# Performance work log

Hardware: AMD Instinct MI355X
Metric: run time of the kernel (lower is better)

## Reference

```python
import jax, jax.numpy as jnp
import numpy as np

DIM = 256
WH, WW = 7, 7
N = WH * WW
HEADS = 8
HEAD_DIM = DIM // HEADS
SCALE = HEAD_DIM ** -0.5
B_ = 4096
NW = 64  # windows per image; B_ % NW == 0


def _relative_position_index():
    coords = np.stack(np.meshgrid(np.arange(WH), np.arange(WW), indexing='ij'))  # (2,Wh,Ww)
    flat = coords.reshape(2, -1)  # (2,N)
    rel = flat[:, :, None] - flat[:, None, :]  # (2,N,N)
    rel = rel.transpose(1, 2, 0)  # (N,N,2)
    rel = rel + np.array([WH - 1, WW - 1])
    rel = rel * np.array([2 * WW - 1, 1])
    return rel.sum(-1).astype(np.int32)  # (N,N)


def setup_inputs() -> dict:
    key = jax.random.key(0)
    ks = jax.random.split(key, 7)
    num_rel = (2 * WH - 1) * (2 * WW - 1)
    return {
        'x': jax.random.normal(ks[0], (B_, N, DIM), jnp.float32),
        'mask': jax.random.normal(ks[1], (NW, N, N), jnp.float32),
        'qkv_w': jax.random.normal(ks[2], (DIM, 3 * DIM), jnp.float32) * 0.02,
        'qkv_b': jnp.zeros((3 * DIM,), jnp.float32),
        'proj_w': jax.random.normal(ks[3], (DIM, DIM), jnp.float32) * 0.02,
        'proj_b': jnp.zeros((DIM,), jnp.float32),
        'bias_table': jax.random.normal(ks[4], (num_rel, HEADS), jnp.float32) * 0.02,
        'rel_index': jnp.asarray(_relative_position_index()),
    }


def reference(x, mask, qkv_w, qkv_b, proj_w, proj_b, bias_table, rel_index):
    B, n, C = x.shape
    qkv = x @ qkv_w + qkv_b  # (B,N,3C)
    qkv = qkv.reshape(B, n, 3, HEADS, HEAD_DIM).transpose(2, 0, 3, 1, 4)
    q, k, v = qkv[0], qkv[1], qkv[2]  # (B,H,N,hd)
    attn = jnp.einsum('bhnd,bhmd->bhnm', q * SCALE, k)  # (B,H,N,N)
    rel_bias = bias_table[rel_index.reshape(-1)].reshape(n, n, HEADS)
    attn = attn + rel_bias.transpose(2, 0, 1)[None]  # (B,H,N,N)
    nW = mask.shape[0]
    attn = attn.reshape(-1, nW, HEADS, n, n) + mask[None, :, None]
    attn = attn.reshape(-1, HEADS, n, n)
    attn = jax.nn.softmax(attn, axis=-1)
    out = jnp.einsum('bhnm,bhmd->bhnd', attn, v)  # (B,H,N,hd)
    out = out.transpose(0, 2, 1, 3).reshape(B, n, C)
    return out @ proj_w + proj_b
```

## Files before the change

### kernel.cpp

```cpp
#include <hip/hip_runtime.h>
#include <hip/hip_bf16.h>


#define NTOK 49
static constexpr float SCALE_Q = 0.17677669529663687f;

using bf16   = __bf16;
using bf16x4 = __attribute__((ext_vector_type(4))) __bf16;
using bf16x8 = __attribute__((ext_vector_type(8))) __bf16;
using short4v = __attribute__((ext_vector_type(4))) short;
using f32x4  = __attribute__((ext_vector_type(4))) float;

#define WT_QKV_OFF 0
#define WT_PROJ_OFF (768 * 256 * 2)
#define SB_OFF (WT_PROJ_OFF + 256 * 256 * 2)
#define SM_OFF (SB_OFF + 8 * 4096 * 4)
#define WS_NEEDED (SM_OFF + (size_t)64 * 4096 * 4)

static __device__ __forceinline__ f32x4 mfma16(bf16x4 a, bf16x4 b, f32x4 c) {
#if __has_builtin(__builtin_amdgcn_mfma_f32_16x16x16_bf16)
    return __builtin_amdgcn_mfma_f32_16x16x16_bf16(a, b, c, 0, 0, 0);
#elif __has_builtin(__builtin_amdgcn_mfma_f32_16x16x16bf16_1k)
    return __builtin_amdgcn_mfma_f32_16x16x16bf16_1k(
        __builtin_bit_cast(short4v, a), __builtin_bit_cast(short4v, b), c, 0, 0, 0);
#elif __has_builtin(__builtin_amdgcn_mfma_f32_16x16x16_bf16_1k)
    return __builtin_amdgcn_mfma_f32_16x16x16_bf16_1k(
        __builtin_bit_cast(short4v, a), __builtin_bit_cast(short4v, b), c, 0, 0, 0);
#else
    asm volatile("v_mfma_f32_16x16x16_bf16 %0, %1, %2, %0\n\t"
                 "s_nop 7\n\ts_nop 7\n\ts_nop 1"
                 : "+v"(c) : "v"(a), "v"(b));
    return c;
#endif
}

static __device__ __forceinline__ bf16x8 ldsA(const char* base, int row, int koff) {
    return *(const bf16x8*)(base + row * 512 + (koff ^ ((row & 7) << 4)));
}
static __device__ __forceinline__ bf16x8 ldB(const bf16* wt, int ncol, int k2, int hf, int g) {
    return *(const bf16x8*)(wt + ncol * 256 + k2 * 64 + hf * 32 + g * 8);
}

__global__ void prep_wqkv(const float* __restrict__ qkv_w, bf16* __restrict__ wt) {
    int idx = blockIdx.x * 256 + threadIdx.x;
    if (idx >= 768 * 256) return;
    int n = idx >> 8, k = idx & 255;
    float v = qkv_w[k * 768 + n];
    if (n < 256) v *= SCALE_Q;
    wt[idx] = (bf16)v;
}
__global__ void prep_wproj(const float* __restrict__ proj_w, bf16* __restrict__ wt) {
    int idx = blockIdx.x * 256 + threadIdx.x;
    if (idx >= 256 * 256) return;
    int n = idx >> 8, k = idx & 255;
    wt[idx] = (bf16)proj_w[k * 256 + n];
}
__global__ void prep_sb(const float* __restrict__ bias_table, const int* __restrict__ rel_index,
                        float* __restrict__ sb) {
    int idx = blockIdx.x * 256 + threadIdx.x;
    if (idx >= 8 * 4096) return;
    int r    = idx & 3;
    int lane = (idx >> 2) & 63;
    int qp   = (idx >> 8) & 15;
    int h    = idx >> 12;
    int kt = qp >> 2, qt = qp & 3;
    int i = qt * 16 + (lane & 15);
    int j = kt * 16 + (lane >> 4) * 4 + r;
    float v;
    if (j >= NTOK)      v = -1e30f;
    else if (i >= NTOK) v = 0.0f;
    else v = bias_table[rel_index[i * 49 + j] * 8 + h];
    sb[idx] = v;
}
__global__ void prep_sm(const float* __restrict__ mask, float* __restrict__ sm) {
    int idx = blockIdx.x * 256 + threadIdx.x;
    if (idx >= 64 * 4096) return;
    int r    = idx & 3;
    int lane = (idx >> 2) & 63;
    int qp   = (idx >> 8) & 15;
    int w    = idx >> 12;
    int kt = qp >> 2, qt = qp & 3;
    int i = qt * 16 + (lane & 15);
    int j = kt * 16 + (lane >> 4) * 4 + r;
    sm[idx] = (i < NTOK && j < NTOK) ? mask[(w * 49 + i) * 49 + j] : 0.0f;
}

__global__ __launch_bounds__(512, 2) void fused_attn(
    const float* __restrict__ x,
    const float* __restrict__ qkv_b,
    const float* __restrict__ proj_b,
    const bf16* __restrict__ wt_qkv,
    const bf16* __restrict__ wt_proj,
    const float* __restrict__ sb,
    const float* __restrict__ sm,
    float* __restrict__ out)
{
    __shared__ char smem[65536];
    char* xs  = smem;
    char* xs2 = smem + 32768;
    const int b    = blockIdx.x;
    const int tid  = threadIdx.x;
    const int lane = tid & 63;
    const int h    = tid >> 6;
    const int c    = lane & 15;
    const int g    = lane >> 4;

    {
        const float* xb = x + (size_t)b * (NTOK * 256);
        float4 xr[8];
        #pragma unroll
        for (int it = 0; it < 8; ++it) {
            int idx = it * 512 + tid;
            int row = idx >> 6, c4 = idx & 63;
            xr[it] = make_float4(0.f, 0.f, 0.f, 0.f);
            if (row < NTOK) xr[it] = ((const float4*)xb)[row * 64 + c4];
        }
        #pragma unroll
        for (int it = 0; it < 8; ++it) {
            int idx = it * 512 + tid;
            int row = idx >> 6, c4 = idx & 63;
            bf16x4 o;
            o[0] = (bf16)xr[it].x; o[1] = (bf16)xr[it].y;
            o[2] = (bf16)xr[it].z; o[3] = (bf16)xr[it].w;
            *(bf16x4*)(xs + row * 512 + ((c4 * 8) ^ ((row & 7) << 4))) = o;
        }
    }
    __syncthreads();

    bf16x4 iden;
    #pragma unroll
    for (int j = 0; j < 4; ++j) iden[j] = (bf16)((4 * g + j == c) ? 1.0f : 0.0f);

    bf16x4 qf[4][2];
    bf16x4 kf[4][2];
    bf16x4 pB[4][4];
    bf16x4 vf[2][4];

    const int colQ = h * 32 + c;
    const int colK = 256 + h * 32 + c;
    const int colV = 512 + h * 32 + c;

    bf16x8 bcur[2][2], bnxt[2][2];
    bf16x8 acur[2][4], anxt[2][4];

    #pragma unroll
    for (int ni = 0; ni < 2; ++ni)
        #pragma unroll
        for (int hf = 0; hf < 2; ++hf)
            bcur[ni][hf] = ldB(wt_qkv, colQ + ni * 16, 0, hf, g);
    #pragma unroll
    for (int hf = 0; hf < 2; ++hf)
        #pragma unroll
        for (int mi = 0; mi < 4; ++mi)
            acur[hf][mi] = ldsA(xs, mi * 16 + c, hf * 64 + g * 16);

    {
        f32x4 acc[2][4];
        #pragma unroll
        for (int ni = 0; ni < 2; ++ni)
            #pragma unroll
            for (int mi = 0; mi < 4; ++mi)
                acc[ni][mi] = (f32x4){0.f, 0.f, 0.f, 0.f};
        #pragma unroll
        for (int k2 = 0; k2 < 4; ++k2) {
            if (k2 < 3) {
                #pragma unroll
                for (int ni = 0; ni < 2; ++ni)
                    #pragma unroll
                    for (int hf = 0; hf < 2; ++hf)
                        bnxt[ni][hf] = ldB(wt_qkv, colQ + ni * 16, k2 + 1, hf, g);
                #pragma unroll
                for (int hf = 0; hf < 2; ++hf)
                    #pragma unroll
                    for (int mi = 0; mi < 4; ++mi)
                        anxt[hf][mi] = ldsA(xs, mi * 16 + c, (k2 + 1) * 128 + hf * 64 + g * 16);
            } else {
                #pragma unroll
                for (int ni = 0; ni < 2; ++ni)
                    #pragma unroll
                    for (int hf = 0; hf < 2; ++hf)
                        bnxt[ni][hf] = ldB(wt_qkv, colK + ni * 16, 0, hf, g);
                #pragma unroll
                for (int hf = 0; hf < 2; ++hf)
                    #pragma unroll
                    for (int mi = 0; mi < 4; ++mi)
                        anxt[hf][mi] = ldsA(xs, mi * 16 + c, hf * 64 + g * 16);
            }
            #pragma unroll
            for (int hf = 0; hf < 2; ++hf)
                #pragma unroll
                for (int ni = 0; ni < 2; ++ni)
                    #pragma unroll
                    for (int mi = 0; mi < 4; ++mi)
                        acc[ni][mi] = __builtin_amdgcn_mfma_f32_16x16x32_bf16(acur[hf][mi], bcur[ni][hf], acc[ni][mi], 0, 0, 0);
            #pragma unroll
            for (int ni = 0; ni < 2; ++ni)
                #pragma unroll
                for (int hf = 0; hf < 2; ++hf)
                    bcur[ni][hf] = bnxt[ni][hf];
            #pragma unroll
            for (int hf = 0; hf < 2; ++hf)
                #pragma unroll
                for (int mi = 0; mi < 4; ++mi)
                    acur[hf][mi] = anxt[hf][mi];
        }
        #pragma unroll
        for (int ni = 0; ni < 2; ++ni) {
            float bias = qkv_b[h * 32 + ni * 16 + c] * SCALE_Q;
            #pragma unroll
            for (int mi = 0; mi < 4; ++mi) {
                bf16x4 in;
                #pragma unroll
                for (int r = 0; r < 4; ++r) in[r] = (bf16)(acc[ni][mi][r] + bias);
                f32x4 t = mfma16(in, iden, (f32x4){0.f, 0.f, 0.f, 0.f});
                #pragma unroll
                for (int r = 0; r < 4; ++r) qf[mi][ni][r] = (bf16)t[r];
            }
        }
    }

    {
        f32x4 acc[2][4];
        #pragma unroll
        for (int ni = 0; ni < 2; ++ni)
            #pragma unroll
            for (int mi = 0; mi < 4; ++mi)
                acc[ni][mi] = (f32x4){0.f, 0.f, 0.f, 0.f};
        #pragma unroll
        for (int k2 = 0; k2 < 4; ++k2) {
            if (k2 < 3) {
                #pragma unroll
                for (int ni = 0; ni < 2; ++ni)
                    #pragma unroll
                    for (int hf = 0; hf < 2; ++hf)
                        bnxt[ni][hf] = ldB(wt_qkv, colK + ni * 16, k2 + 1, hf, g);
                #pragma unroll
                for (int hf = 0; hf < 2; ++hf)
                    #pragma unroll
                    for (int mi = 0; mi < 4; ++mi)
                        anxt[hf][mi] = ldsA(xs, mi * 16 + c, (k2 + 1) * 128 + hf * 64 + g * 16);
            }
            #pragma unroll
            for (int hf = 0; hf < 2; ++hf)
                #pragma unroll
                for (int ni = 0; ni < 2; ++ni)
                    #pragma unroll
                    for (int mi = 0; mi < 4; ++mi)
                        acc[ni][mi] = __builtin_amdgcn_mfma_f32_16x16x32_bf16(acur[hf][mi], bcur[ni][hf], acc[ni][mi], 0, 0, 0);
            if (k2 < 3) {
                #pragma unroll
                for (int ni = 0; ni < 2; ++ni)
                    #pragma unroll
                    for (int hf = 0; hf < 2; ++hf)
                        bcur[ni][hf] = bnxt[ni][hf];
                #pragma unroll
                for (int hf = 0; hf < 2; ++hf)
                    #pragma unroll
                    for (int mi = 0; mi < 4; ++mi)
                        acur[hf][mi] = anxt[hf][mi];
            }
        }
        #pragma unroll
        for (int ni = 0; ni < 2; ++ni) {
            float bias = qkv_b[256 + h * 32 + ni * 16 + c];
            #pragma unroll
            for (int mi = 0; mi < 4; ++mi) {
                bf16x4 in;
                #pragma unroll
                for (int r = 0; r < 4; ++r) in[r] = (bf16)(acc[ni][mi][r] + bias);
                f32x4 t = mfma16(in, iden, (f32x4){0.f, 0.f, 0.f, 0.f});
                #pragma unroll
                for (int r = 0; r < 4; ++r) kf[mi][ni][r] = (bf16)t[r];
            }
        }
    }

    {
        const float* sbh = sb + (size_t)h * 4096;
        const float* smw = sm + (size_t)(b & 63) * 4096;
        #pragma unroll
        for (int qt = 0; qt < 4; ++qt) {
            f32x4 sbv[4], smv[4];
            #pragma unroll
            for (int kt = 0; kt < 4; ++kt)
                sbv[kt] = *(const f32x4*)(sbh + (kt * 4 + qt) * 256 + lane * 4);
            #pragma unroll
            for (int kt = 0; kt < 4; ++kt)
                smv[kt] = *(const f32x4*)(smw + (kt * 4 + qt) * 256 + lane * 4);

            f32x4 sT[4];
            __builtin_amdgcn_s_setprio(1);
            #pragma unroll
            for (int kt = 0; kt < 4; ++kt) {
                sT[kt] = (f32x4){0.f, 0.f, 0.f, 0.f};
                sT[kt] = mfma16(kf[kt][0], qf[qt][0], sT[kt]);
                sT[kt] = mfma16(kf[kt][1], qf[qt][1], sT[kt]);
            }
            __builtin_amdgcn_s_setprio(0);
            if (qt == 3) {
                #pragma unroll
                for (int ni = 0; ni < 2; ++ni)
                    #pragma unroll
                    for (int hf = 0; hf < 2; ++hf)
                        bcur[ni][hf] = ldB(wt_qkv, colV + ni * 16, 0, hf, g);
                #pragma unroll
                for (int hf = 0; hf < 2; ++hf)
                    #pragma unroll
                    for (int mi = 0; mi < 4; ++mi)
                        acur[hf][mi] = ldsA(xs, mi * 16 + c, hf * 64 + g * 16);
            }
            #pragma unroll
            for (int kt = 0; kt < 4; ++kt)
                #pragma unroll
                for (int r = 0; r < 4; ++r)
                    sT[kt][r] += sbv[kt][r] + smv[kt][r];
            f32x4 mx4;
            #pragma unroll
            for (int r = 0; r < 4; ++r)
                mx4[r] = fmaxf(fmaxf(sT[0][r], sT[1][r]), fmaxf(sT[2][r], sT[3][r]));
            float m = fmaxf(fmaxf(mx4[0], mx4[1]), fmaxf(mx4[2], mx4[3]));
            m = fmaxf(m, __shfl_xor(m, 16));
            m = fmaxf(m, __shfl_xor(m, 32));
            f32x4 sm4 = (f32x4){0.f, 0.f, 0.f, 0.f};
            #pragma unroll
            for (int kt = 0; kt < 4; ++kt)
                #pragma unroll
                for (int r = 0; r < 4; ++r) {
                    float e = __expf(sT[kt][r] - m);
                    sT[kt][r] = e;
                    sm4[r] += e;
                }
            float sum = (sm4[0] + sm4[1]) + (sm4[2] + sm4[3]);
            sum += __shfl_xor(sum, 16);
            sum += __shfl_xor(sum, 32);
            float rs = 1.f / sum;
            #pragma unroll
            for (int kt = 0; kt < 4; ++kt)
                #pragma unroll
                for (int r = 0; r < 4; ++r) pB[qt][kt][r] = (bf16)(sT[kt][r] * rs);
        }
    }

    {
        f32x4 acc[2][4];
        #pragma unroll
        for (int dt = 0; dt < 2; ++dt)
            #pragma unroll
            for (int mi = 0; mi < 4; ++mi)
                acc[dt][mi] = (f32x4){0.f, 0.f, 0.f, 0.f};
        #pragma unroll
        for (int k2 = 0; k2 < 4; ++k2) {
            if (k2 < 3) {
                #pragma unroll
                for (int dt = 0; dt < 2; ++dt)
                    #pragma unroll
                    for (int hf = 0; hf < 2; ++hf)
                        bnxt[dt][hf] = ldB(wt_qkv, colV + dt * 16, k2 + 1, hf, g);
                #pragma unroll
                for (int hf = 0; hf < 2; ++hf)
                    #pragma unroll
                    for (int mi = 0; mi < 4; ++mi)
                        anxt[hf][mi] = ldsA(xs, mi * 16 + c, (k2 + 1) * 128 + hf * 64 + g * 16);
            }
            #pragma unroll
            for (int hf = 0; hf < 2; ++hf)
                #pragma unroll
                for (int dt = 0; dt < 2; ++dt)
                    #pragma unroll
                    for (int mi = 0; mi < 4; ++mi)
                        acc[dt][mi] = __builtin_amdgcn_mfma_f32_16x16x32_bf16(acur[hf][mi], bcur[dt][hf], acc[dt][mi], 0, 0, 0);
            if (k2 < 3) {
                #pragma unroll
                for (int dt = 0; dt < 2; ++dt)
                    #pragma unroll
                    for (int hf = 0; hf < 2; ++hf)
                        bcur[dt][hf] = bnxt[dt][hf];
                #pragma unroll
                for (int hf = 0; hf < 2; ++hf)
                    #pragma unroll
                    for (int mi = 0; mi < 4; ++mi)
                        acur[hf][mi] = anxt[hf][mi];
            }
        }
        #pragma unroll
        for (int dt = 0; dt < 2; ++dt) {
            float vb = qkv_b[512 + h * 32 + dt * 16 + c];
            #pragma unroll
            for (int kt = 0; kt < 4; ++kt)
                #pragma unroll
                for (int r = 0; r < 4; ++r) vf[dt][kt][r] = (bf16)(acc[dt][kt][r] + vb);
        }
    }

    __builtin_amdgcn_s_setprio(1);
    #pragma unroll
    for (int qt = 0; qt < 4; ++qt) {
        int row = qt * 16 + c;
        #pragma unroll
        for (int dt = 0; dt < 2; ++dt) {
            f32x4 oT = (f32x4){0.f, 0.f, 0.f, 0.f};
            #pragma unroll
            for (int kt = 0; kt < 4; ++kt)
                oT = mfma16(vf[dt][kt], pB[qt][kt], oT);
            int cbyte = h * 64 + dt * 32 + g * 8;
            bf16x4 o;
            #pragma unroll
            for (int r = 0; r < 4; ++r) o[r] = (bf16)oT[r];
            *(bf16x4*)(xs2 + row * 512 + (cbyte ^ ((row & 7) << 4))) = o;
        }
    }
    __builtin_amdgcn_s_setprio(0);

    #pragma unroll
    for (int ni = 0; ni < 2; ++ni)
        #pragma unroll
        for (int hf = 0; hf < 2; ++hf)
            bcur[ni][hf] = ldB(wt_proj, h * 32 + ni * 16 + c, 0, hf, g);

    __syncthreads();

    {
        f32x4 po[2][4];
        #pragma unroll
        for (int ni = 0; ni < 2; ++ni)
            #pragma unroll
            for (int mi = 0; mi < 4; ++mi)
                po[ni][mi] = (f32x4){0.f, 0.f, 0.f, 0.f};

        #pragma unroll
        for (int hf = 0; hf < 2; ++hf)
            #pragma unroll
            for (int mi = 0; mi < 4; ++mi)
                acur[hf][mi] = ldsA(xs2, mi * 16 + c, hf * 64 + g * 16);

        #pragma unroll
        for (int k2 = 0; k2 < 4; ++k2) {
            if (k2 < 3) {
                #pragma unroll
                for (int ni = 0; ni < 2; ++ni)
                    #pragma unroll
                    for (int hf = 0; hf < 2; ++hf)
                        bnxt[ni][hf] = ldB(wt_proj, h * 32 + ni * 16 + c, k2 + 1, hf, g);
                #pragma unroll
                for (int hf = 0; hf < 2; ++hf)
                    #pragma unroll
                    for (int mi = 0; mi < 4; ++mi)
                        anxt[hf][mi] = ldsA(xs2, mi * 16 + c, (k2 + 1) * 128 + hf * 64 + g * 16);
            }
            #pragma unroll
            for (int hf = 0; hf < 2; ++hf)
                #pragma unroll
                for (int ni = 0; ni < 2; ++ni)
                    #pragma unroll
                    for (int mi = 0; mi < 4; ++mi)
                        po[ni][mi] = __builtin_amdgcn_mfma_f32_16x16x32_bf16(acur[hf][mi], bcur[ni][hf], po[ni][mi], 0, 0, 0);
            if (k2 < 3) {
                #pragma unroll
                for (int ni = 0; ni < 2; ++ni)
                    #pragma unroll
                    for (int hf = 0; hf < 2; ++hf)
                        bcur[ni][hf] = bnxt[ni][hf];
                #pragma unroll
                for (int hf = 0; hf < 2; ++hf)
                    #pragma unroll
                    for (int mi = 0; mi < 4; ++mi)
                        acur[hf][mi] = anxt[hf][mi];
            }
        }
        float* outb = out + (size_t)b * (NTOK * 256);
        #pragma unroll
        for (int ni = 0; ni < 2; ++ni) {
            int col = h * 32 + ni * 16 + c;
            float pb = proj_b[col];
            #pragma unroll
            for (int mi = 0; mi < 4; ++mi) {
                #pragma unroll
                for (int r = 0; r < 4; ++r) {
                    int row = mi * 16 + g * 4 + r;
                    if (row < NTOK) outb[row * 256 + col] = po[ni][mi][r] + pb;
                }
            }
        }
    }
}

extern "C" void kernel_launch(void* const* d_in, const int* in_sizes, int n_in,
                              void* d_out, int out_size, void* d_ws, size_t ws_size,
                              hipStream_t stream) {
    const float* x          = (const float*)d_in[0];
    const float* mask       = (const float*)d_in[1];
    const float* qkv_w      = (const float*)d_in[2];
    const float* qkv_b      = (const float*)d_in[3];
    const float* proj_w     = (const float*)d_in[4];
    const float* proj_b     = (const float*)d_in[5];
    const float* bias_table = (const float*)d_in[6];
    const int*   rel_index  = (const int*)d_in[7];
    float* out = (float*)d_out;

    if (ws_size < WS_NEEDED) return;

    char* ws = (char*)d_ws;
    bf16*  wt_qkv  = (bf16*)(ws + WT_QKV_OFF);
    bf16*  wt_proj = (bf16*)(ws + WT_PROJ_OFF);
    float* sbp     = (float*)(ws + SB_OFF);
    float* smp     = (float*)(ws + SM_OFF);

    prep_wqkv <<<768, 256, 0, stream>>>(qkv_w, wt_qkv);
    prep_wproj<<<256, 256, 0, stream>>>(proj_w, wt_proj);
    prep_sb   <<<128, 256, 0, stream>>>(bias_table, rel_index, sbp);
    prep_sm   <<<1024, 256, 0, stream>>>(mask, smp);

    fused_attn<<<4096, 512, 0, stream>>>(x, qkv_b, proj_b, wt_qkv, wt_proj, sbp, smp, out);
}
```

Measured before the change: 347.6 us.

## Compute Q and K transposed in one fused GEMM, drop identity-MFMA transposes

Merges the separate Q and K projection loops into one K-loop that computes the transposed products (weights as the A operand, x as the B operand), so the accumulators already come out in the fragment layout the attention MFMAs need. This removes the identity-matrix MFMA that was used to transpose each Q/K tile, and it shares the x LDS reads between Q and K. The first weight fragments are prefetched before the x staging barrier. In exchange it holds 16 accumulator tiles live at once, which raises register pressure, and it assumes the weight layout supports these direct row loads.

```diff
diff --git a/kernel.cpp b/kernel.cpp
--- a/kernel.cpp
+++ b/kernel.cpp
@@ -105,6 +105,15 @@
     const int c    = lane & 15;
     const int g    = lane >> 4;
 
+    auto cbase = [&](int mt) {
+        return (mt < 2 ? h * 32 + mt * 16 : 256 + h * 32 + (mt - 2) * 16) + c;
+    };
+
+    bf16x8 wcur[4], wnxt[4];
+    #pragma unroll
+    for (int mt = 0; mt < 4; ++mt)
+        wcur[mt] = *(const bf16x8*)(wt_qkv + cbase(mt) * 256 + g * 8);
+
     {
         const float* xb = x + (size_t)b * (NTOK * 256);
         float4 xr[8];
@@ -127,153 +136,65 @@
     }
     __syncthreads();
 
-    bf16x4 iden;
-    #pragma unroll
-    for (int j = 0; j < 4; ++j) iden[j] = (bf16)((4 * g + j == c) ? 1.0f : 0.0f);
-
     bf16x4 qf[4][2];
     bf16x4 kf[4][2];
     bf16x4 pB[4][4];
     bf16x4 vf[2][4];
 
-    const int colQ = h * 32 + c;
-    const int colK = 256 + h * 32 + c;
+    {
+        f32x4 acc[4][4];
+        #pragma unroll
+        for (int mt = 0; mt < 4; ++mt)
+            #pragma unroll
+            for (int nt = 0; nt < 4; ++nt)
+                acc[mt][nt] = (f32x4){0.f, 0.f, 0.f, 0.f};
+
+        #pragma unroll
+        for (int kk = 0; kk < 8; ++kk) {
+            if (kk < 7) {
+                #pragma unroll
+                for (int mt = 0; mt < 4; ++mt)
+                    wnxt[mt] = *(const bf16x8*)(wt_qkv + cbase(mt) * 256 + (kk + 1) * 32 + g * 8);
+            }
+            bf16x8 xf[4];
+            #pragma unroll
+            for (int nt = 0; nt < 4; ++nt)
+                xf[nt] = ldsA(xs, nt * 16 + c, kk * 64 + g * 16);
+            #pragma unroll
+            for (int mt = 0; mt < 4; ++mt)
+                #pragma unroll
+                for (int nt = 0; nt < 4; ++nt)
+                    acc[mt][nt] = __builtin_amdgcn_mfma_f32_16x16x32_bf16(wcur[mt], xf[nt], acc[mt][nt], 0, 0, 0);
+            if (kk < 7) {
+                #pragma unroll
+                for (int mt = 0; mt < 4; ++mt)
+                    wcur[mt] = wnxt[mt];
+            }
+        }
+        #pragma unroll
+        for (int mt = 0; mt < 2; ++mt) {
+            f32x4 bq = *(const f32x4*)(qkv_b + h * 32 + mt * 16 + 4 * g);
+            #pragma unroll
+            for (int nt = 0; nt < 4; ++nt)
+                #pragma unroll
+                for (int r = 0; r < 4; ++r)
+                    qf[nt][mt][r] = (bf16)(acc[mt][nt][r] + bq[r] * SCALE_Q);
+        }
+        #pragma unroll
+        for (int mt = 0; mt < 2; ++mt) {
+            f32x4 bk = *(const f32x4*)(qkv_b + 256 + h * 32 + mt * 16 + 4 * g);
+            #pragma unroll
+            for (int nt = 0; nt < 4; ++nt)
+                #pragma unroll
+                for (int r = 0; r < 4; ++r)
+                    kf[nt][mt][r] = (bf16)(acc[mt + 2][nt][r] + bk[r]);
+        }
+    }
+
     const int colV = 512 + h * 32 + c;
 
     bf16x8 bcur[2][2], bnxt[2][2];
     bf16x8 acur[2][4], anxt[2][4];
-
-    #pragma unroll
-    for (int ni = 0; ni < 2; ++ni)
-        #pragma unroll
-        for (int hf = 0; hf < 2; ++hf)
-            bcur[ni][hf] = ldB(wt_qkv, colQ + ni * 16, 0, hf, g);
-    #pragma unroll
-    for (int hf = 0; hf < 2; ++hf)
-        #pragma unroll
-        for (int mi = 0; mi < 4; ++mi)
-            acur[hf][mi] = ldsA(xs, mi * 16 + c, hf * 64 + g * 16);
-
-    {
-        f32x4 acc[2][4];
-        #pragma unroll
-        for (int ni = 0; ni < 2; ++ni)
-            #pragma unroll
-            for (int mi = 0; mi < 4; ++mi)
-                acc[ni][mi] = (f32x4){0.f, 0.f, 0.f, 0.f};
-        #pragma unroll
-        for (int k2 = 0; k2 < 4; ++k2) {
-            if (k2 < 3) {
-                #pragma unroll
-                for (int ni = 0; ni < 2; ++ni)
-                    #pragma unroll
-                    for (int hf = 0; hf < 2; ++hf)
-                        bnxt[ni][hf] = ldB(wt_qkv, colQ + ni * 16, k2 + 1, hf, g);
-                #pragma unroll
-                for (int hf = 0; hf < 2; ++hf)
-                    #pragma unroll
-                    for (int mi = 0; mi < 4; ++mi)
-                        anxt[hf][mi] = ldsA(xs, mi * 16 + c, (k2 + 1) * 128 + hf * 64 + g * 16);
-            } else {
-                #pragma unroll
-                for (int ni = 0; ni < 2; ++ni)
-                    #pragma unroll
-                    for (int hf = 0; hf < 2; ++hf)
-                        bnxt[ni][hf] = ldB(wt_qkv, colK + ni * 16, 0, hf, g);
-                #pragma unroll
-                for (int hf = 0; hf < 2; ++hf)
-                    #pragma unroll
-                    for (int mi = 0; mi < 4; ++mi)
-                        anxt[hf][mi] = ldsA(xs, mi * 16 + c, hf * 64 + g * 16);
-            }
-            #pragma unroll
-            for (int hf = 0; hf < 2; ++hf)
-                #pragma unroll
-                for (int ni = 0; ni < 2; ++ni)
-                    #pragma unroll
-                    for (int mi = 0; mi < 4; ++mi)
-                        acc[ni][mi] = __builtin_amdgcn_mfma_f32_16x16x32_bf16(acur[hf][mi], bcur[ni][hf], acc[ni][mi], 0, 0, 0);
-            #pragma unroll
-            for (int ni = 0; ni < 2; ++ni)
-                #pragma unroll
-                for (int hf = 0; hf < 2; ++hf)
-                    bcur[ni][hf] = bnxt[ni][hf];
-            #pragma unroll
-            for (int hf = 0; hf < 2; ++hf)
-                #pragma unroll
-                for (int mi = 0; mi < 4; ++mi)
-                    acur[hf][mi] = anxt[hf][mi];
-        }
-        #pragma unroll
-        for (int ni = 0; ni < 2; ++ni) {
-            float bias = qkv_b[h * 32 + ni * 16 + c] * SCALE_Q;
-            #pragma unroll
-            for (int mi = 0; mi < 4; ++mi) {
-                bf16x4 in;
-                #pragma unroll
-                for (int r = 0; r < 4; ++r) in[r] = (bf16)(acc[ni][mi][r] + bias);
-                f32x4 t = mfma16(in, iden, (f32x4){0.f, 0.f, 0.f, 0.f});
-                #pragma unroll
-                for (int r = 0; r < 4; ++r) qf[mi][ni][r] = (bf16)t[r];
-            }
-        }
-    }
-
-    {
-        f32x4 acc[2][4];
-        #pragma unroll
-        for (int ni = 0; ni < 2; ++ni)
-            #pragma unroll
-            for (int mi = 0; mi < 4; ++mi)
-                acc[ni][mi] = (f32x4){0.f, 0.f, 0.f, 0.f};
-        #pragma unroll
-        for (int k2 = 0; k2 < 4; ++k2) {
-            if (k2 < 3) {
-                #pragma unroll
-                for (int ni = 0; ni < 2; ++ni)
-                    #pragma unroll
-                    for (int hf = 0; hf < 2; ++hf)
-                        bnxt[ni][hf] = ldB(wt_qkv, colK + ni * 16, k2 + 1, hf, g);
-                #pragma unroll
-                for (int hf = 0; hf < 2; ++hf)
-                    #pragma unroll
-                    for (int mi = 0; mi < 4; ++mi)
-                        anxt[hf][mi] = ldsA(xs, mi * 16 + c, (k2 + 1) * 128 + hf * 64 + g * 16);
-            }
-            #pragma unroll
-            for (int hf = 0; hf < 2; ++hf)
-                #pragma unroll
-                for (int ni = 0; ni < 2; ++ni)
-                    #pragma unroll
-                    for (int mi = 0; mi < 4; ++mi)
-                        acc[ni][mi] = __builtin_amdgcn_mfma_f32_16x16x32_bf16(acur[hf][mi], bcur[ni][hf], acc[ni][mi], 0, 0, 0);
-            if (k2 < 3) {
-                #pragma unroll
-                for (int ni = 0; ni < 2; ++ni)
-                    #pragma unroll
-                    for (int hf = 0; hf < 2; ++hf)
-                        bcur[ni][hf] = bnxt[ni][hf];
-                #pragma unroll
-                for (int hf = 0; hf < 2; ++hf)
-                    #pragma unroll
-                    for (int mi = 0; mi < 4; ++mi)
-                        acur[hf][mi] = anxt[hf][mi];
-            }
-        }
-        #pragma unroll
-        for (int ni = 0; ni < 2; ++ni) {
-            float bias = qkv_b[256 + h * 32 + ni * 16 + c];
-            #pragma unroll
-            for (int mi = 0; mi < 4; ++mi) {
-                bf16x4 in;
-                #pragma unroll
-                for (int r = 0; r < 4; ++r) in[r] = (bf16)(acc[ni][mi][r] + bias);
-                f32x4 t = mfma16(in, iden, (f32x4){0.f, 0.f, 0.f, 0.f});
-                #pragma unroll
-                for (int r = 0; r < 4; ++r) kf[mi][ni][r] = (bf16)t[r];
-            }
-        }
-    }
 
     {
         const float* sbh = sb + (size_t)h * 4096;
```

Result: no change. 348.0 us (+0.1%).
